# Performance work log

Measured on AMD Instinct MI355X. Metric: run time of the kernel, lower is better.

## Reference

```python
import jax, jax.numpy as jnp
import numpy as np


def setup_inputs() -> dict:
    key = jax.random.key(0)
    ks = jax.random.split(key, 8)
    B, N, E, F = 8, 200, 128, 16
    scale = 0.05
    return {
        "h": jax.random.normal(ks[0], (B, N, E), dtype=jnp.float32),
        "edge_features": jax.random.normal(ks[1], (B, N, N, F), dtype=jnp.float32),
        "W": jax.random.uniform(ks[2], (B, N, N), dtype=jnp.float32),
        "W_node": jax.random.normal(ks[3], (E, E), dtype=jnp.float32) * scale,
        "W_edge": jax.random.normal(ks[4], (E, F), dtype=jnp.float32) * scale,
        "W_weight": jax.random.normal(ks[5], (E, 1), dtype=jnp.float32) * scale,
        "W_out": jax.random.normal(ks[6], (E, E), dtype=jnp.float32) * scale,
        "b_out": jax.random.normal(ks[7], (E,), dtype=jnp.float32) * scale,
    }


def reference(h, edge_features, W, W_node, W_edge, W_weight, W_out, b_out):
    # hi: [B,N,1,E]  (node_proj)
    hi = jnp.einsum('bne,fe->bnf', h, W_node)[:, :, None, :]
    # ej: [B,N,N,E]  (edge_proj)
    ej = jnp.einsum('bnmf,ef->bnme', edge_features, W_edge)
    # wij: [B,N,N,E] (weight_proj of scalar W)
    wij = W[..., None] * W_weight[:, 0]  # broadcast [B,N,N,1]*[E]
    msg = jnp.tanh(hi + ej + wij)        # [B,N,N,E]
    agg = msg.mean(axis=2)               # [B,N,E]
    return jnp.einsum('bne,fe->bnf', agg, W_out) + b_out
```

## Files before the change

kernel.cpp:

```cpp
#include <hip/hip_runtime.h>

typedef __attribute__((ext_vector_type(4))) float  f32x4;
typedef __attribute__((ext_vector_type(8))) short  short8;
typedef __attribute__((ext_vector_type(4))) unsigned int u32x4;
typedef __attribute__((ext_vector_type(2))) unsigned int u32x2;

#define NN 200
#define EDIM 128
#define FDIM 16
#define BN_TOTAL 1600
#define NCHUNK 7
#define MSG_BLOCKS 2800
#define LAMBDA 2.8853900817779268f

#define WS_WOUT_S 2176
#define WSF_HI    10240
#define WSF_PART  215040

__device__ __forceinline__ unsigned short f2bf(float f) {
    unsigned u = __float_as_uint(f);
    u += 0x7FFFu + ((u >> 16) & 1u);
    return (unsigned short)(u >> 16);
}
__device__ __forceinline__ short8 cvt8(f32x4 a, f32x4 b) {
    short8 r;
    r[0]=(short)f2bf(a.x); r[1]=(short)f2bf(a.y); r[2]=(short)f2bf(a.z); r[3]=(short)f2bf(a.w);
    r[4]=(short)f2bf(b.x); r[5]=(short)f2bf(b.y); r[6]=(short)f2bf(b.z); r[7]=(short)f2bf(b.w);
    return r;
}
__device__ __forceinline__ unsigned cvtpk(float lo, float hi) {
    unsigned r;
    asm("v_cvt_pk_bf16_f32 %0, %1, %2" : "=v"(r) : "v"(lo), "v"(hi));
    return r;
}
__device__ __forceinline__ float sigr(float x) {
    return __builtin_amdgcn_rcpf(1.0f + __builtin_amdgcn_exp2f(x));
}

__global__ __launch_bounds__(128) void setup_kernel(
    const float* __restrict__ h, const float* __restrict__ W_node,
    const float* __restrict__ W_edge, const float* __restrict__ W_weight,
    const float* __restrict__ W_out,
    unsigned short* __restrict__ wcvt,
    unsigned short* __restrict__ wout,
    float* __restrict__ hi_arr)
{
    const int blk = blockIdx.x;
    const int tid = threadIdx.x;

    if (blk < 200) {
        const int rb   = blk >> 1;
        const int eh   = blk & 1;
        const int lane = tid & 63;
        const int w    = tid >> 6;
        const int g    = lane >> 4;
        const int l15  = lane & 15;
        const int r0   = rb * 16;

        short8 afr[4];
#pragma unroll
        for (int ks = 0; ks < 4; ++ks) {
            const float* p = h + (size_t)(r0 + l15) * EDIM + ks * 32 + g * 8;
            afr[ks] = cvt8(*(const f32x4*)p, *(const f32x4*)(p + 4));
        }
#pragma unroll
        for (int e2 = 0; e2 < 2; ++e2) {
            const int et = eh * 4 + w * 2 + e2;
            f32x4 acc = {0.f, 0.f, 0.f, 0.f};
#pragma unroll
            for (int ks = 0; ks < 4; ++ks) {
                const float* p = W_node + (size_t)(et * 16 + l15) * EDIM + ks * 32 + g * 8;
                short8 bfr = cvt8(*(const f32x4*)p, *(const f32x4*)(p + 4));
                acc = __builtin_amdgcn_mfma_f32_16x16x32_bf16(afr[ks], bfr, acc, 0, 0, 0);
            }
#pragma unroll
            for (int r = 0; r < 4; ++r)
                hi_arr[(size_t)(r0 + g * 4 + r) * EDIM + et * 16 + l15] = acc[r] * LAMBDA;
        }
    } else {
        for (int c = (blk - 200) * 128 + tid; c < 4640; c += 8 * 128) {
            const float* src; unsigned short* dst; float sc;
            if (c < 512)      { src = W_edge   + c * 4;         dst = wcvt + c * 4;               sc = LAMBDA; }
            else if (c < 544) { src = W_weight + (c - 512) * 4; dst = wcvt + 2048 + (c - 512) * 4; sc = LAMBDA; }
            else              { src = W_out    + (c - 544) * 4; dst = wout + (c - 544) * 4;        sc = 1.0f; }
            f32x4 v = *(const f32x4*)src;
            v.x *= sc; v.y *= sc; v.z *= sc; v.w *= sc;
            u32x2 pk = { (unsigned)f2bf(v.x) | ((unsigned)f2bf(v.y) << 16),
                         (unsigned)f2bf(v.z) | ((unsigned)f2bf(v.w) << 16) };
            *(u32x2*)dst = pk;
        }
    }
}

#define LOAD_ITEM(BE, BH, BN, CJ)                                             \
  do {                                                                        \
    _Pragma("unroll")                                                         \
    for (int t_ = 0; t_ < 2; ++t_) {                                          \
      int row_  = (CJ) * 32 + t_ * 16 + l15;                                  \
      int rowc_ = row_ > NN - 1 ? NN - 1 : row_;                              \
      if (g < 2) {                                                            \
        const float* p_ = ef + ((size_t)(BN) * NN + rowc_) * FDIM + g * 8;    \
        BE[t_ * 2]     = *(const f32x4*)p_;                                   \
        BE[t_ * 2 + 1] = *(const f32x4*)(p_ + 4);                             \
      } else if (g == 2) {                                                    \
        BE[t_ * 2].x = Wadj[(BN) * NN + rowc_];                               \
      }                                                                       \
    }                                                                         \
    _Pragma("unroll")                                                         \
    for (int et_ = 0; et_ < 8; ++et_)                                         \
      BH[et_] = hi_arr[(size_t)(BN) * EDIM + et_ * 16 + l15];                 \
  } while (0)

#define COMP_ITEM(BE, BH, BN, CJ)                                             \
  do {                                                                        \
    float Sr_[8];                                                             \
    _Pragma("unroll")                                                         \
    for (int et_ = 0; et_ < 8; ++et_) Sr_[et_] = 0.f;                         \
    _Pragma("unroll")                                                         \
    for (int t_ = 0; t_ < 2; ++t_) {                                          \
      short8 a_;                                                              \
      if (g < 2) {                                                            \
        u32x4 pk_ = { cvtpk(BE[t_*2].x,   BE[t_*2].y),                        \
                      cvtpk(BE[t_*2].z,   BE[t_*2].w),                        \
                      cvtpk(BE[t_*2+1].x, BE[t_*2+1].y),                      \
                      cvtpk(BE[t_*2+1].z, BE[t_*2+1].w) };                    \
        a_ = __builtin_bit_cast(short8, pk_);                                 \
      } else {                                                                \
        short8 z_ = {0,0,0,0,0,0,0,0};                                        \
        if (g == 2) {                                                         \
          z_[0] = (short)f2bf(BE[t_*2].x);                                    \
          if ((CJ) * 32 + t_ * 16 + l15 >= NN) z_[1] = (short)0x4980;         \
        }                                                                     \
        a_ = z_;                                                              \
      }                                                                       \
      _Pragma("unroll")                                                       \
      for (int et_ = 0; et_ < 8; ++et_) {                                     \
        f32x4 c_ = {BH[et_], BH[et_], BH[et_], BH[et_]};                      \
        c_ = __builtin_amdgcn_mfma_f32_16x16x32_bf16(a_, bfrag[et_], c_, 0, 0, 0); \
        Sr_[et_] += sigr(c_[0]) + sigr(c_[1]) + sigr(c_[2]) + sigr(c_[3]);    \
      }                                                                       \
    }                                                                         \
    _Pragma("unroll")                                                         \
    for (int et_ = 0; et_ < 8; ++et_) {                                       \
      float p_ = Sr_[et_];                                                    \
      p_ += __shfl_xor(p_, 16);                                               \
      p_ += __shfl_xor(p_, 32);                                               \
      Sr_[et_] = p_;                                                          \
    }                                                                         \
    if (g == 0) {                                                             \
      float* dst_ = part + ((size_t)(CJ) * BN_TOTAL + (BN)) * EDIM + l15;     \
      _Pragma("unroll")                                                       \
      for (int et_ = 0; et_ < 8; ++et_) dst_[et_ * 16] = Sr_[et_];            \
    }                                                                         \
  } while (0)

__global__ __launch_bounds__(64) void msg_kernel(
    const float* __restrict__ ef, const float* __restrict__ Wadj,
    const unsigned short* __restrict__ wcvt,
    const float* __restrict__ hi_arr,
    float* __restrict__ part)
{
    const int lane = threadIdx.x;
    const int g    = lane >> 4;
    const int l15  = lane & 15;

    short8 bfrag[8];
#pragma unroll
    for (int et = 0; et < 8; ++et) {
        short8 b = {0, 0, 0, 0, 0, 0, 0, 0};
        if (g < 2) b = *(const short8*)(wcvt + (et * 16 + l15) * FDIM + g * 8);
        else if (g == 2) {
            b[0] = (short)wcvt[2048 + et * 16 + l15];
            b[1] = (short)0x4980;
        }
        bfrag[et] = b;
    }

    const int idx = blockIdx.x * 4;
    int bn_[4], cj_[4];
#pragma unroll
    for (int k = 0; k < 4; ++k) {
        int id = idx + k;
        int b  = (id * 18725) >> 17;
        bn_[k] = b; cj_[k] = id - b * 7;
    }

    f32x4 beA[4], beB[4];
    float bhA[8], bhB[8];

    LOAD_ITEM(beA, bhA, bn_[0], cj_[0]);
    LOAD_ITEM(beB, bhB, bn_[1], cj_[1]);
    COMP_ITEM(beA, bhA, bn_[0], cj_[0]);
    LOAD_ITEM(beA, bhA, bn_[2], cj_[2]);
    COMP_ITEM(beB, bhB, bn_[1], cj_[1]);
    LOAD_ITEM(beB, bhB, bn_[3], cj_[3]);
    COMP_ITEM(beA, bhA, bn_[2], cj_[2]);
    COMP_ITEM(beB, bhB, bn_[3], cj_[3]);
}

__global__ __launch_bounds__(128) void outproj_kernel(
    const float* __restrict__ part, const unsigned short* __restrict__ wout,
    const float* __restrict__ b_out, float* __restrict__ out)
{
    const int tid  = threadIdx.x;
    const int lane = tid & 63;
    const int w    = tid >> 6;
    const int g    = lane >> 4;
    const int l15  = lane & 15;
    const int rb   = blockIdx.x >> 1;
    const int fh   = blockIdx.x & 1;
    const int r0   = rb * 16;

    short8 afr[4];
#pragma unroll
    for (int ks = 0; ks < 4; ++ks) {
        const size_t off = (size_t)(r0 + l15) * EDIM + ks * 32 + g * 8;
        f32x4 s0 = {0.f, 0.f, 0.f, 0.f}, s1 = {0.f, 0.f, 0.f, 0.f};
#pragma unroll
        for (int j = 0; j < NCHUNK; ++j) {
            const float* p = part + (size_t)j * (BN_TOTAL * EDIM) + off;
            s0 += *(const f32x4*)p;
            s1 += *(const f32x4*)(p + 4);
        }
        f32x4 a0, a1;
        a0.x = __builtin_fmaf(-0.01f, s0.x, 1.0f);
        a0.y = __builtin_fmaf(-0.01f, s0.y, 1.0f);
        a0.z = __builtin_fmaf(-0.01f, s0.z, 1.0f);
        a0.w = __builtin_fmaf(-0.01f, s0.w, 1.0f);
        a1.x = __builtin_fmaf(-0.01f, s1.x, 1.0f);
        a1.y = __builtin_fmaf(-0.01f, s1.y, 1.0f);
        a1.z = __builtin_fmaf(-0.01f, s1.z, 1.0f);
        a1.w = __builtin_fmaf(-0.01f, s1.w, 1.0f);
        afr[ks] = cvt8(a0, a1);
    }
#pragma unroll
    for (int f2 = 0; f2 < 2; ++f2) {
        const int ft = fh * 4 + w * 2 + f2;
        f32x4 acc = {0.f, 0.f, 0.f, 0.f};
#pragma unroll
        for (int ks = 0; ks < 4; ++ks) {
            short8 b = *(const short8*)(wout + (ft * 16 + l15) * EDIM + ks * 32 + g * 8);
            acc = __builtin_amdgcn_mfma_f32_16x16x32_bf16(afr[ks], b, acc, 0, 0, 0);
        }
        const float bo = b_out[ft * 16 + l15];
#pragma unroll
        for (int r = 0; r < 4; ++r)
            out[(size_t)(r0 + g * 4 + r) * EDIM + ft * 16 + l15] = acc[r] + bo;
    }
}

extern "C" void kernel_launch(void* const* d_in, const int* in_sizes, int n_in,
                              void* d_out, int out_size, void* d_ws, size_t ws_size,
                              hipStream_t stream) {
    const float* h        = (const float*)d_in[0];
    const float* ef       = (const float*)d_in[1];
    const float* W        = (const float*)d_in[2];
    const float* W_node   = (const float*)d_in[3];
    const float* W_edge   = (const float*)d_in[4];
    const float* W_weight = (const float*)d_in[5];
    const float* W_out    = (const float*)d_in[6];
    const float* b_out    = (const float*)d_in[7];
    float* out = (float*)d_out;

    unsigned short* wsb = (unsigned short*)d_ws;
    float*          wsf = (float*)d_ws;
    unsigned short* wcvt   = wsb;
    unsigned short* wout   = wsb + WS_WOUT_S;
    float*          hi_arr = wsf + WSF_HI;
    float*          part   = wsf + WSF_PART;

    setup_kernel<<<208, 128, 0, stream>>>(h, W_node, W_edge, W_weight, W_out,
                                          wcvt, wout, hi_arr);
    msg_kernel<<<MSG_BLOCKS, 64, 0, stream>>>(ef, W, wcvt, hi_arr, part);
    outproj_kernel<<<200, 128, 0, stream>>>(part, wout, b_out, out);
}
```

Baseline: 37.35 us.

## Split msg kernel's four work items across four waves per block

The message kernel previously ran one 64-thread wave per block that software-pipelined four (bn, chunk) items through two register buffers. Now each block has four waves, and each wave handles one item with no manual load/compute interleaving. The aim is more waves in flight, so latency is hidden by occupancy instead of explicit pipelining. In exchange, each wave reloads the B fragments and the intra-wave load/compute overlap is gone.

```diff
diff --git a/kernel.cpp b/kernel.cpp
--- a/kernel.cpp
+++ b/kernel.cpp
@@ -10,7 +10,6 @@
 #define FDIM 16
 #define BN_TOTAL 1600
 #define NCHUNK 7
-#define MSG_BLOCKS 2800
 #define LAMBDA 2.8853900817779268f
 
 #define WS_WOUT_S 2176
@@ -92,77 +91,39 @@
     }
 }
 
-#define LOAD_ITEM(BE, BH, BN, CJ)                                             \
-  do {                                                                        \
-    _Pragma("unroll")                                                         \
-    for (int t_ = 0; t_ < 2; ++t_) {                                          \
-      int row_  = (CJ) * 32 + t_ * 16 + l15;                                  \
-      int rowc_ = row_ > NN - 1 ? NN - 1 : row_;                              \
-      if (g < 2) {                                                            \
-        const float* p_ = ef + ((size_t)(BN) * NN + rowc_) * FDIM + g * 8;    \
-        BE[t_ * 2]     = *(const f32x4*)p_;                                   \
-        BE[t_ * 2 + 1] = *(const f32x4*)(p_ + 4);                             \
-      } else if (g == 2) {                                                    \
-        BE[t_ * 2].x = Wadj[(BN) * NN + rowc_];                               \
-      }                                                                       \
-    }                                                                         \
-    _Pragma("unroll")                                                         \
-    for (int et_ = 0; et_ < 8; ++et_)                                         \
-      BH[et_] = hi_arr[(size_t)(BN) * EDIM + et_ * 16 + l15];                 \
-  } while (0)
-
-#define COMP_ITEM(BE, BH, BN, CJ)                                             \
-  do {                                                                        \
-    float Sr_[8];                                                             \
-    _Pragma("unroll")                                                         \
-    for (int et_ = 0; et_ < 8; ++et_) Sr_[et_] = 0.f;                         \
-    _Pragma("unroll")                                                         \
-    for (int t_ = 0; t_ < 2; ++t_) {                                          \
-      short8 a_;                                                              \
-      if (g < 2) {                                                            \
-        u32x4 pk_ = { cvtpk(BE[t_*2].x,   BE[t_*2].y),                        \
-                      cvtpk(BE[t_*2].z,   BE[t_*2].w),                        \
-                      cvtpk(BE[t_*2+1].x, BE[t_*2+1].y),                      \
-                      cvtpk(BE[t_*2+1].z, BE[t_*2+1].w) };                    \
-        a_ = __builtin_bit_cast(short8, pk_);                                 \
-      } else {                                                                \
-        short8 z_ = {0,0,0,0,0,0,0,0};                                        \
-        if (g == 2) {                                                         \
-          z_[0] = (short)f2bf(BE[t_*2].x);                                    \
-          if ((CJ) * 32 + t_ * 16 + l15 >= NN) z_[1] = (short)0x4980;         \
-        }                                                                     \
-        a_ = z_;                                                              \
-      }                                                                       \
-      _Pragma("unroll")                                                       \
-      for (int et_ = 0; et_ < 8; ++et_) {                                     \
-        f32x4 c_ = {BH[et_], BH[et_], BH[et_], BH[et_]};                      \
-        c_ = __builtin_amdgcn_mfma_f32_16x16x32_bf16(a_, bfrag[et_], c_, 0, 0, 0); \
-        Sr_[et_] += sigr(c_[0]) + sigr(c_[1]) + sigr(c_[2]) + sigr(c_[3]);    \
-      }                                                                       \
-    }                                                                         \
-    _Pragma("unroll")                                                         \
-    for (int et_ = 0; et_ < 8; ++et_) {                                       \
-      float p_ = Sr_[et_];                                                    \
-      p_ += __shfl_xor(p_, 16);                                               \
-      p_ += __shfl_xor(p_, 32);                                               \
-      Sr_[et_] = p_;                                                          \
-    }                                                                         \
-    if (g == 0) {                                                             \
-      float* dst_ = part + ((size_t)(CJ) * BN_TOTAL + (BN)) * EDIM + l15;     \
-      _Pragma("unroll")                                                       \
-      for (int et_ = 0; et_ < 8; ++et_) dst_[et_ * 16] = Sr_[et_];            \
-    }                                                                         \
-  } while (0)
-
-__global__ __launch_bounds__(64) void msg_kernel(
+__global__ __launch_bounds__(256, 5) void msg_kernel(
     const float* __restrict__ ef, const float* __restrict__ Wadj,
     const unsigned short* __restrict__ wcvt,
     const float* __restrict__ hi_arr,
     float* __restrict__ part)
 {
-    const int lane = threadIdx.x;
+    const int tid  = threadIdx.x;
+    const int lane = tid & 63;
+    const int wid  = tid >> 6;
     const int g    = lane >> 4;
     const int l15  = lane & 15;
+
+    const int id = blockIdx.x * 4 + wid;
+    const int bn = (id * 18725) >> 17;
+    const int cj = id - bn * 7;
+
+    f32x4 be[4];
+#pragma unroll
+    for (int t = 0; t < 2; ++t) {
+        int row  = cj * 32 + t * 16 + l15;
+        int rowc = row > NN - 1 ? NN - 1 : row;
+        if (g < 2) {
+            const float* p = ef + ((size_t)bn * NN + rowc) * FDIM + g * 8;
+            be[t * 2]     = *(const f32x4*)p;
+            be[t * 2 + 1] = *(const f32x4*)(p + 4);
+        } else if (g == 2) {
+            be[t * 2].x = Wadj[bn * NN + rowc];
+        }
+    }
+    float bh[8];
+#pragma unroll
+    for (int et = 0; et < 8; ++et)
+        bh[et] = hi_arr[(size_t)bn * EDIM + et * 16 + l15];
 
     short8 bfrag[8];
 #pragma unroll
@@ -176,26 +137,47 @@
         bfrag[et] = b;
     }
 
-    const int idx = blockIdx.x * 4;
-    int bn_[4], cj_[4];
-#pragma unroll
-    for (int k = 0; k < 4; ++k) {
-        int id = idx + k;
-        int b  = (id * 18725) >> 17;
-        bn_[k] = b; cj_[k] = id - b * 7;
-    }
-
-    f32x4 beA[4], beB[4];
-    float bhA[8], bhB[8];
-
-    LOAD_ITEM(beA, bhA, bn_[0], cj_[0]);
-    LOAD_ITEM(beB, bhB, bn_[1], cj_[1]);
-    COMP_ITEM(beA, bhA, bn_[0], cj_[0]);
-    LOAD_ITEM(beA, bhA, bn_[2], cj_[2]);
-    COMP_ITEM(beB, bhB, bn_[1], cj_[1]);
-    LOAD_ITEM(beB, bhB, bn_[3], cj_[3]);
-    COMP_ITEM(beA, bhA, bn_[2], cj_[2]);
-    COMP_ITEM(beB, bhB, bn_[3], cj_[3]);
+    float Sr[8];
+#pragma unroll
+    for (int et = 0; et < 8; ++et) Sr[et] = 0.f;
+
+#pragma unroll
+    for (int t = 0; t < 2; ++t) {
+        short8 a;
+        if (g < 2) {
+            u32x4 pk = { cvtpk(be[t*2].x,   be[t*2].y),
+                         cvtpk(be[t*2].z,   be[t*2].w),
+                         cvtpk(be[t*2+1].x, be[t*2+1].y),
+                         cvtpk(be[t*2+1].z, be[t*2+1].w) };
+            a = __builtin_bit_cast(short8, pk);
+        } else {
+            short8 z = {0,0,0,0,0,0,0,0};
+            if (g == 2) {
+                z[0] = (short)f2bf(be[t*2].x);
+                if (cj * 32 + t * 16 + l15 >= NN) z[1] = (short)0x4980;
+            }
+            a = z;
+        }
+#pragma unroll
+        for (int et = 0; et < 8; ++et) {
+            f32x4 c = {bh[et], bh[et], bh[et], bh[et]};
+            c = __builtin_amdgcn_mfma_f32_16x16x32_bf16(a, bfrag[et], c, 0, 0, 0);
+            Sr[et] += sigr(c[0]) + sigr(c[1]) + sigr(c[2]) + sigr(c[3]);
+        }
+    }
+
+#pragma unroll
+    for (int et = 0; et < 8; ++et) {
+        float p = Sr[et];
+        p += __shfl_xor(p, 16);
+        p += __shfl_xor(p, 32);
+        Sr[et] = p;
+    }
+    if (g == 0) {
+        float* dst = part + ((size_t)cj * BN_TOTAL + bn) * EDIM + l15;
+#pragma unroll
+        for (int et = 0; et < 8; ++et) dst[et * 16] = Sr[et];
+    }
 }
 
 __global__ __launch_bounds__(128) void outproj_kernel(
@@ -271,6 +253,6 @@
 
     setup_kernel<<<208, 128, 0, stream>>>(h, W_node, W_edge, W_weight, W_out,
                                           wcvt, wout, hi_arr);
-    msg_kernel<<<MSG_BLOCKS, 64, 0, stream>>>(ef, W, wcvt, hi_arr, part);
+    msg_kernel<<<2800, 256, 0, stream>>>(ef, W, wcvt, hi_arr, part);
     outproj_kernel<<<200, 128, 0, stream>>>(part, wout, b_out, out);
 }
```

Measured after the change: 48.59 us. 1.3x slower.

## Coalesce partial-sum stores and restructure outproj to one row per block

Applied to the files above, without the earlier changes.

The message kernel now has all 64 lanes write the reduced partial sums as two contiguous 64-float rows. Before, only the first 16-lane group wrote, with strided stores. The output projection launches one 64-thread block per (b,n) row instead of 16-row tiles. Each block reads its row contiguously, broadcasts values into MFMA A fragments with shuffles, and writes one coalesced output row. This raises block count and coalescing but leaves 15 of 16 MFMA rows redundant, and each block re-reads the full bf16 W_out from cache.

```diff
diff --git a/kernel.cpp b/kernel.cpp
--- a/kernel.cpp
+++ b/kernel.cpp
@@ -147,10 +147,12 @@
       p_ += __shfl_xor(p_, 32);                                               \
       Sr_[et_] = p_;                                                          \
     }                                                                         \
-    if (g == 0) {                                                             \
-      float* dst_ = part + ((size_t)(CJ) * BN_TOTAL + (BN)) * EDIM + l15;     \
-      _Pragma("unroll")                                                       \
-      for (int et_ = 0; et_ < 8; ++et_) dst_[et_ * 16] = Sr_[et_];            \
+    {                                                                         \
+      float v0_ = (g == 0) ? Sr_[0] : (g == 1) ? Sr_[1] : (g == 2) ? Sr_[2] : Sr_[3]; \
+      float v1_ = (g == 0) ? Sr_[4] : (g == 1) ? Sr_[5] : (g == 2) ? Sr_[6] : Sr_[7]; \
+      float* dst_ = part + ((size_t)(CJ) * BN_TOTAL + (BN)) * EDIM;           \
+      dst_[lane]      = v0_;                                                  \
+      dst_[64 + lane] = v1_;                                                  \
     }                                                                         \
   } while (0)
 
@@ -198,55 +200,58 @@
     COMP_ITEM(beB, bhB, bn_[3], cj_[3]);
 }
 
-__global__ __launch_bounds__(128) void outproj_kernel(
+__global__ __launch_bounds__(64) void outproj_kernel(
     const float* __restrict__ part, const unsigned short* __restrict__ wout,
     const float* __restrict__ b_out, float* __restrict__ out)
 {
-    const int tid  = threadIdx.x;
-    const int lane = tid & 63;
-    const int w    = tid >> 6;
+    const int lane = threadIdx.x;
     const int g    = lane >> 4;
     const int l15  = lane & 15;
-    const int rb   = blockIdx.x >> 1;
-    const int fh   = blockIdx.x & 1;
-    const int r0   = rb * 16;
-
-    short8 afr[4];
+    const int bn   = blockIdx.x;
+
+    float s0 = 0.f, s1 = 0.f;
+#pragma unroll
+    for (int j = 0; j < NCHUNK; ++j) {
+        const float* p = part + ((size_t)j * BN_TOTAL + bn) * EDIM;
+        s0 += p[lane];
+        s1 += p[64 + lane];
+    }
+    const float a0 = __builtin_fmaf(-0.01f, s0, 1.0f);
+    const float a1 = __builtin_fmaf(-0.01f, s1, 1.0f);
+
+    short8 af[4];
 #pragma unroll
     for (int ks = 0; ks < 4; ++ks) {
-        const size_t off = (size_t)(r0 + l15) * EDIM + ks * 32 + g * 8;
-        f32x4 s0 = {0.f, 0.f, 0.f, 0.f}, s1 = {0.f, 0.f, 0.f, 0.f};
-#pragma unroll
-        for (int j = 0; j < NCHUNK; ++j) {
-            const float* p = part + (size_t)j * (BN_TOTAL * EDIM) + off;
-            s0 += *(const f32x4*)p;
-            s1 += *(const f32x4*)(p + 4);
-        }
-        f32x4 a0, a1;
-        a0.x = __builtin_fmaf(-0.01f, s0.x, 1.0f);
-        a0.y = __builtin_fmaf(-0.01f, s0.y, 1.0f);
-        a0.z = __builtin_fmaf(-0.01f, s0.z, 1.0f);
-        a0.w = __builtin_fmaf(-0.01f, s0.w, 1.0f);
-        a1.x = __builtin_fmaf(-0.01f, s1.x, 1.0f);
-        a1.y = __builtin_fmaf(-0.01f, s1.y, 1.0f);
-        a1.z = __builtin_fmaf(-0.01f, s1.z, 1.0f);
-        a1.w = __builtin_fmaf(-0.01f, s1.w, 1.0f);
-        afr[ks] = cvt8(a0, a1);
-    }
-#pragma unroll
-    for (int f2 = 0; f2 < 2; ++f2) {
-        const int ft = fh * 4 + w * 2 + f2;
+        const float src = (ks < 2) ? a0 : a1;
+        const int base = (ks & 1) * 32 + g * 8;
+        float t0 = __shfl(src, base + 0, 64);
+        float t1 = __shfl(src, base + 1, 64);
+        float t2 = __shfl(src, base + 2, 64);
+        float t3 = __shfl(src, base + 3, 64);
+        float t4 = __shfl(src, base + 4, 64);
+        float t5 = __shfl(src, base + 5, 64);
+        float t6 = __shfl(src, base + 6, 64);
+        float t7 = __shfl(src, base + 7, 64);
+        u32x4 pk = { cvtpk(t0, t1), cvtpk(t2, t3), cvtpk(t4, t5), cvtpk(t6, t7) };
+        af[ks] = __builtin_bit_cast(short8, pk);
+    }
+
+    float o[8];
+#pragma unroll
+    for (int ft = 0; ft < 8; ++ft) {
         f32x4 acc = {0.f, 0.f, 0.f, 0.f};
 #pragma unroll
         for (int ks = 0; ks < 4; ++ks) {
             short8 b = *(const short8*)(wout + (ft * 16 + l15) * EDIM + ks * 32 + g * 8);
-            acc = __builtin_amdgcn_mfma_f32_16x16x32_bf16(afr[ks], b, acc, 0, 0, 0);
-        }
-        const float bo = b_out[ft * 16 + l15];
-#pragma unroll
-        for (int r = 0; r < 4; ++r)
-            out[(size_t)(r0 + g * 4 + r) * EDIM + ft * 16 + l15] = acc[r] + bo;
-    }
+            acc = __builtin_amdgcn_mfma_f32_16x16x32_bf16(af[ks], b, acc, 0, 0, 0);
+        }
+        o[ft] = acc[0];
+    }
+
+    const float v0 = (g == 0) ? o[0] : (g == 1) ? o[1] : (g == 2) ? o[2] : o[3];
+    const float v1 = (g == 0) ? o[4] : (g == 1) ? o[5] : (g == 2) ? o[6] : o[7];
+    out[(size_t)bn * EDIM + lane]      = v0 + b_out[lane];
+    out[(size_t)bn * EDIM + 64 + lane] = v1 + b_out[64 + lane];
 }
 
 extern "C" void kernel_launch(void* const* d_in, const int* in_sizes, int n_in,
@@ -272,5 +277,5 @@
     setup_kernel<<<208, 128, 0, stream>>>(h, W_node, W_edge, W_weight, W_out,
                                           wcvt, wout, hi_arr);
     msg_kernel<<<MSG_BLOCKS, 64, 0, stream>>>(ef, W, wcvt, hi_arr, part);
-    outproj_kernel<<<200, 128, 0, stream>>>(part, wout, b_out, out);
-}
+    outproj_kernel<<<BN_TOTAL, 64, 0, stream>>>(part, wout, b_out, out);
+}
```

Result: slower. 38.70 us (+3.6%).
